# Kernel tuning notes

Hardware: AMD Instinct MI355X
Metric: run time of the kernel (lower is better)

The kernel has to match this reference:

```python
import jax, jax.numpy as jnp
import numpy as np

B, S, H, NH = 8, 1024, 1024, 16
DH = H // NH


def setup_inputs() -> dict:
    key = jax.random.key(0)
    ks = jax.random.split(key, 16)
    inp = {
        'v': jax.random.normal(ks[0], (B, S, H), jnp.float32),
        'k': jax.random.normal(ks[1], (B, S, H), jnp.float32),
        'q': jax.random.normal(ks[2], (B, S, H), jnp.float32),
        'r': jax.random.normal(ks[3], (B, S, H), jnp.float32),
        'mask': jax.random.randint(ks[4], (B, 1, 1, S), 0, 2).astype(jnp.bool_),
    }
    scale = 1.0 / np.sqrt(H)
    names = ['Wv', 'Wk', 'Wq', 'Wr', 'Wm']
    for i, n in enumerate(names):
        inp[n] = jax.random.normal(ks[5 + i], (H, H), jnp.float32) * scale
        inp['b' + n[1:]] = jnp.zeros((H,), jnp.float32)
    return inp


def _heads(x, W, b):
    # torch Linear: x @ W.T + b, then split heads -> [B, NH, S, DH]
    y = jnp.einsum('bsh,oh->bso', x, W) + b
    return y.reshape(B, S, NH, DH).transpose(0, 2, 1, 3)


def reference(v, k, q, r, mask, Wv, bv, Wk, bk, Wq, bq, Wr, br, Wm, bm):
    vh = _heads(v, Wv, bv)
    kh = _heads(k, Wk, bk)
    qh = _heads(q, Wq, bq)
    rh = _heads(r, Wr, br)
    # relation-augmented scores: (QK^T + RK^T) / sqrt(d_k)
    scores = jnp.einsum('bhqd,bhkd->bhqk', qh + rh, kh) / jnp.sqrt(jnp.asarray(DH, qh.dtype))
    scores = jnp.where(mask, jnp.asarray(-1e9, scores.dtype), scores)
    att = jax.nn.softmax(scores, axis=-1)  # dropout = identity in eval
    out = jnp.einsum('bhqk,bhkd->bhqd', att, vh)
    out = out.transpose(0, 2, 1, 3).reshape(B, S, H)
    return jnp.einsum('bsh,oh->bso', out, Wm) + bm
```

## Files before the change

kernel.cpp:

```cpp
#include <hip/hip_runtime.h>
#include <hip/hip_bf16.h>
#include <stdint.h>

typedef __attribute__((ext_vector_type(4))) float f32x4;
typedef __attribute__((ext_vector_type(8))) short s16x8;
typedef __attribute__((ext_vector_type(4))) short s16x4;
typedef __attribute__((ext_vector_type(4))) int i32x4;

typedef const __attribute__((address_space(1))) unsigned glb_u32;
typedef __attribute__((address_space(3))) unsigned lds_u32;

#define DEVI __device__ __forceinline__

DEVI short f2b(float f) {
    union { float f; unsigned u; } v; v.f = f;
    unsigned r = v.u + 0x7fffu + ((v.u >> 16) & 1u);
    return (short)(r >> 16);
}

struct Ptr5 { const float* p[5]; };
struct Ptr4 { const float* p[4]; };

__global__ __launch_bounds__(256) void cvtW(Ptr5 src, short* __restrict__ dst) {
    const float* s = src.p[blockIdx.y];
    short* d = dst + (size_t)blockIdx.y * (1024u * 1024u);
    int i = (blockIdx.x * 256 + threadIdx.x) * 8;
    f32x4 a = *(const f32x4*)(s + i);
    f32x4 b = *(const f32x4*)(s + i + 4);
    s16x8 o;
#pragma unroll
    for (int j = 0; j < 4; ++j) { o[j] = f2b(a[j]); o[4 + j] = f2b(b[j]); }
    *(s16x8*)(d + i) = o;
}

__global__ __launch_bounds__(256) void cvtA(Ptr4 src, short* __restrict__ dst) {
    const float* s = src.p[blockIdx.y];
    short* d = dst + (size_t)blockIdx.y * (8u * 1024u * 1024u);
    int i = (blockIdx.x * 256 + threadIdx.x) * 8;
    f32x4 a = *(const f32x4*)(s + i);
    f32x4 b = *(const f32x4*)(s + i + 4);
    s16x8 o;
#pragma unroll
    for (int j = 0; j < 4; ++j) { o[j] = f2b(a[j]); o[4 + j] = f2b(b[j]); }
    *(s16x8*)(d + i) = o;
}

template<int AF32, int OUTMODE, int TWO>
__global__ __launch_bounds__(256) void gemm_nt(
    const void* __restrict__ A0_, const void* __restrict__ A1_,
    const short* __restrict__ W0, const short* __restrict__ W1,
    const float* __restrict__ b0, const float* __restrict__ b1,
    void* __restrict__ C_)
{
    constexpr int K = 1024, N = 1024;
    const int tid = threadIdx.x;
    const int lane = tid & 63, wid = tid >> 6;
    const int wm = wid >> 1, wn = wid & 1;
    const int r = lane & 15, g = lane >> 4;

    const int bid = blockIdx.x;
    const int logical = (bid & 7) * 64 + (bid >> 3);
    const int n0 = (logical & 7) * 128, m0 = (logical >> 3) * 128;

    __shared__ alignas(16) short As[2][128 * 32];
    __shared__ alignas(16) short Ws[2][128 * 32];

    auto stage_async = [&](int buf, int kt) {
        int kk = kt * 32;
        const short* Ap = (const short*)A0_; const short* Wp = W0;
        if (TWO && kk >= 1024) { Ap = (const short*)A1_; Wp = W1; kk &= 1023; }
#pragma unroll
        for (int i = 0; i < 2; ++i) {
            int row = wid * 32 + i * 16 + (lane >> 2);
            const short* ga = Ap + (size_t)(m0 + row) * K + kk + (lane & 3) * 8;
            const short* gw = Wp + (size_t)(n0 + row) * K + kk + (lane & 3) * 8;
            __builtin_amdgcn_global_load_lds((glb_u32*)ga,
                (lds_u32*)&As[buf][(wid * 32 + i * 16) * 32], 16, 0, 0);
            __builtin_amdgcn_global_load_lds((glb_u32*)gw,
                (lds_u32*)&Ws[buf][(wid * 32 + i * 16) * 32], 16, 0, 0);
        }
    };

    const int srow = tid >> 1, shalf = tid & 1;
    f32x4 a0g, a1g, a2g, a3g;
    s16x8 wg0, wg1;
    auto load_regs = [&](int kt) {
        int kk = kt * 32;
        const short* wp = W0 + (size_t)(n0 + srow) * K + kk + shalf * 16;
        wg0 = *(const s16x8*)wp;
        wg1 = *(const s16x8*)(wp + 8);
        const float* ap = (const float*)A0_ + (size_t)(m0 + srow) * K + kk + shalf * 16;
        a0g = *(const f32x4*)ap;       a1g = *(const f32x4*)(ap + 4);
        a2g = *(const f32x4*)(ap + 8); a3g = *(const f32x4*)(ap + 12);
    };
    auto store_lds = [&](int buf) {
        s16x8 s0, s1;
#pragma unroll
        for (int j = 0; j < 4; ++j) {
            s0[j] = f2b(a0g[j]); s0[4 + j] = f2b(a1g[j]);
            s1[j] = f2b(a2g[j]); s1[4 + j] = f2b(a3g[j]);
        }
        char* ab = (char*)As[buf];
        *(s16x8*)(ab + srow * 64 + shalf * 32) = s0;
        *(s16x8*)(ab + srow * 64 + shalf * 32 + 16) = s1;
        char* wb = (char*)Ws[buf];
        *(s16x8*)(wb + srow * 64 + shalf * 32) = wg0;
        *(s16x8*)(wb + srow * 64 + shalf * 32 + 16) = wg1;
    };

    f32x4 z = {0.f, 0.f, 0.f, 0.f};
    f32x4 acc[4][4];
#pragma unroll
    for (int i = 0; i < 4; ++i)
#pragma unroll
        for (int j = 0; j < 4; ++j) acc[i][j] = z;

    auto compute = [&](int buf) {
        s16x8 af[4], bfr[4];
#pragma unroll
        for (int f = 0; f < 4; ++f) {
            af[f]  = *(const s16x8*)&As[buf][(wm * 64 + f * 16 + r) * 32 + g * 8];
            bfr[f] = *(const s16x8*)&Ws[buf][(wn * 64 + f * 16 + r) * 32 + g * 8];
        }
#pragma unroll
        for (int i = 0; i < 4; ++i)
#pragma unroll
            for (int j = 0; j < 4; ++j)
                acc[i][j] = __builtin_amdgcn_mfma_f32_16x16x32_bf16(af[i], bfr[j], acc[i][j], 0, 0, 0);
    };

    constexpr int NK = TWO ? 64 : 32;
    if constexpr (AF32) { load_regs(0); store_lds(0); }
    else stage_async(0, 0);
    __syncthreads();
    int buf = 0;
    for (int kt = 0; kt < NK; ++kt) {
        if (kt + 1 < NK) {
            if constexpr (AF32) load_regs(kt + 1);
            else stage_async(buf ^ 1, kt + 1);
        }
        compute(buf);
        if (AF32 && kt + 1 < NK) store_lds(buf ^ 1);
        __syncthreads();
        buf ^= 1;
    }

#pragma unroll
    for (int j = 0; j < 4; ++j) {
        int col = n0 + wn * 64 + j * 16 + r;
        float bb = b0[col];
        if (TWO) bb += b1[col];
#pragma unroll
        for (int i = 0; i < 4; ++i) {
            int rowb = m0 + wm * 64 + i * 16 + g * 4;
            if constexpr (OUTMODE == 2) {
                int bb_ = rowb >> 10, tok = rowb & 1023;
                short* dst = (short*)C_ + ((size_t)(bb_ * 16 + (col >> 6))) * 65536
                           + (size_t)(col & 63) * 1024 + tok;
                s16x4 o;
#pragma unroll
                for (int q = 0; q < 4; ++q) o[q] = f2b(acc[i][j][q] + bb);
                *(s16x4*)dst = o;
            } else {
#pragma unroll
                for (int q = 0; q < 4; ++q) {
                    float val = acc[i][j][q] + bb;
                    if constexpr (OUTMODE == 1)
                        ((float*)C_)[(size_t)(rowb + q) * N + col] = val;
                    else
                        ((short*)C_)[(size_t)(rowb + q) * N + col] = f2b(val);
                }
            }
        }
    }
}

__global__ __launch_bounds__(256) void attn_fwd(
    const short* __restrict__ qrh, const short* __restrict__ kh,
    const short* __restrict__ vT, const int* __restrict__ mask,
    short* __restrict__ outp)
{
    const int bh = blockIdx.x;
    const int b = bh >> 4, h = bh & 15;
    const int qt = blockIdx.y;
    const int tid = threadIdx.x, lane = tid & 63, wid = tid >> 6;
    const int r = lane & 15, g = lane >> 4;

    __shared__ alignas(16) short Ks[64 * 64];
    __shared__ alignas(16) short Vs[64 * 64];
    __shared__ alignas(16) float mb[1024];

    {
        i32x4 mi = *(const i32x4*)(mask + b * 1024 + tid * 4);
        f32x4 mv;
#pragma unroll
        for (int j = 0; j < 4; ++j) mv[j] = mi[j] ? -1e9f : 0.f;
        *(f32x4*)&mb[tid * 4] = mv;
    }

    const int q0 = qt * 128 + wid * 32;
    const short* qbA = qrh + (size_t)(b * 1024 + q0 + r) * 1024 + h * 64;
    const short* qbB = qbA + 16 * 1024;
    s16x8 qA0 = *(const s16x8*)(qbA + g * 8);
    s16x8 qA1 = *(const s16x8*)(qbA + 32 + g * 8);
    s16x8 qB0 = *(const s16x8*)(qbB + g * 8);
    s16x8 qB1 = *(const s16x8*)(qbB + 32 + g * 8);

    f32x4 z = {0.f, 0.f, 0.f, 0.f};
    f32x4 oA[4], oB[4];
#pragma unroll
    for (int i = 0; i < 4; ++i) { oA[i] = z; oB[i] = z; }
    float mA = -1e30f, mB = -1e30f, lA = 0.f, lB = 0.f;

    const int srow = tid >> 2, sq = tid & 3;
    const short* kg = kh + (size_t)(b * 1024 + srow) * 1024 + h * 64 + sq * 16;
    const short* vg = vT + ((size_t)(b * 16 + h)) * 65536 + (size_t)srow * 1024 + sq * 16;
    const int p0s = (sq * 2) ^ (srow & 7), p1s = (sq * 2 + 1) ^ (srow & 7);

    s16x8 kr0, kr1, vr0, vr1;
    auto stage_load = [&](int t) {
        const short* kp = kg + (size_t)(t * 64) * 1024;
        kr0 = *(const s16x8*)kp; kr1 = *(const s16x8*)(kp + 8);
        const short* vp = vg + t * 64;
        vr0 = *(const s16x8*)vp; vr1 = *(const s16x8*)(vp + 8);
    };
    auto stage_write = [&]() {
        char* kb2 = (char*)Ks;
        *(s16x8*)(kb2 + srow * 128 + p0s * 16) = kr0;
        *(s16x8*)(kb2 + srow * 128 + p1s * 16) = kr1;
        char* vb2 = (char*)Vs;
        *(s16x8*)(vb2 + srow * 128 + p0s * 16) = vr0;
        *(s16x8*)(vb2 + srow * 128 + p1s * 16) = vr1;
    };

    stage_load(0);
    for (int t = 0; t < 16; ++t) {
        if (t) __syncthreads();
        stage_write();
        __syncthreads();
        if (t < 15) stage_load(t + 1);

        f32x4 pA[4], pB[4];
        float tmA = -3e38f, tmB = -3e38f;
        char* kb2 = (char*)Ks;
#pragma unroll
        for (int fn = 0; fn < 4; ++fn) {
            int row = fn * 16 + r;
            s16x8 kfa = *(const s16x8*)(kb2 + row * 128 + ((g ^ (row & 7)) << 4));
            s16x8 kfb = *(const s16x8*)(kb2 + row * 128 + (((4 + g) ^ (row & 7)) << 4));
            f32x4 cA = __builtin_amdgcn_mfma_f32_16x16x32_bf16(kfa, qA0, z, 0, 0, 0);
            cA = __builtin_amdgcn_mfma_f32_16x16x32_bf16(kfb, qA1, cA, 0, 0, 0);
            f32x4 cB = __builtin_amdgcn_mfma_f32_16x16x32_bf16(kfa, qB0, z, 0, 0, 0);
            cB = __builtin_amdgcn_mfma_f32_16x16x32_bf16(kfb, qB1, cB, 0, 0, 0);
            f32x4 mv = *(const f32x4*)&mb[t * 64 + fn * 16 + g * 4];
#pragma unroll
            for (int qi = 0; qi < 4; ++qi) {
                float sA = cA[qi] * 0.125f + mv[qi];
                float sB = cB[qi] * 0.125f + mv[qi];
                pA[fn][qi] = sA; pB[fn][qi] = sB;
                tmA = fmaxf(tmA, sA); tmB = fmaxf(tmB, sB);
            }
        }
        tmA = fmaxf(tmA, __shfl_xor(tmA, 16)); tmA = fmaxf(tmA, __shfl_xor(tmA, 32));
        tmB = fmaxf(tmB, __shfl_xor(tmB, 16)); tmB = fmaxf(tmB, __shfl_xor(tmB, 32));

        float mnA = fmaxf(mA, tmA), mnB = fmaxf(mB, tmB);
        float cA_ = __expf(mA - mnA), cB_ = __expf(mB - mnB);
        mA = mnA; mB = mnB;
        float tsA = 0.f, tsB = 0.f;
#pragma unroll
        for (int fn = 0; fn < 4; ++fn)
#pragma unroll
            for (int qi = 0; qi < 4; ++qi) {
                float eA = __expf(pA[fn][qi] - mA); pA[fn][qi] = eA; tsA += eA;
                float eB = __expf(pB[fn][qi] - mB); pB[fn][qi] = eB; tsB += eB;
            }
        tsA += __shfl_xor(tsA, 16); tsA += __shfl_xor(tsA, 32);
        tsB += __shfl_xor(tsB, 16); tsB += __shfl_xor(tsB, 32);
        lA = lA * cA_ + tsA; lB = lB * cB_ + tsB;
#pragma unroll
        for (int df = 0; df < 4; ++df)
#pragma unroll
            for (int qi = 0; qi < 4; ++qi) { oA[df][qi] *= cA_; oB[df][qi] *= cB_; }

        char* vb2 = (char*)Vs;
#pragma unroll
        for (int ks = 0; ks < 2; ++ks) {
            s16x8 pbA, pbB;
#pragma unroll
            for (int j = 0; j < 4; ++j) {
                pbA[j]     = f2b(pA[2 * ks][j]);
                pbA[4 + j] = f2b(pA[2 * ks + 1][j]);
                pbB[j]     = f2b(pB[2 * ks][j]);
                pbB[4 + j] = f2b(pB[2 * ks + 1][j]);
            }
#pragma unroll
            for (int df = 0; df < 4; ++df) {
                int row = df * 16 + r;
                int sl0 = ks * 4 + (g >> 1), half = (g & 1) * 8;
                s16x4 va0 = *(const s16x4*)(vb2 + row * 128 + ((sl0 ^ (row & 7)) << 4) + half);
                s16x4 va1 = *(const s16x4*)(vb2 + row * 128 + (((sl0 + 2) ^ (row & 7)) << 4) + half);
                s16x8 vf = {va0[0], va0[1], va0[2], va0[3], va1[0], va1[1], va1[2], va1[3]};
                oA[df] = __builtin_amdgcn_mfma_f32_16x16x32_bf16(vf, pbA, oA[df], 0, 0, 0);
                oB[df] = __builtin_amdgcn_mfma_f32_16x16x32_bf16(vf, pbB, oB[df], 0, 0, 0);
            }
        }
    }

    float ivA = 1.f / lA, ivB = 1.f / lB;
#pragma unroll
    for (int df = 0; df < 4; ++df) {
        s16x4 oa, ob;
#pragma unroll
        for (int qi = 0; qi < 4; ++qi) {
            oa[qi] = f2b(oA[df][qi] * ivA);
            ob[qi] = f2b(oB[df][qi] * ivB);
        }
        *(s16x4*)&outp[(size_t)(b * 1024 + q0 + r) * 1024 + h * 64 + df * 16 + g * 4] = oa;
        *(s16x4*)&outp[(size_t)(b * 1024 + q0 + 16 + r) * 1024 + h * 64 + df * 16 + g * 4] = ob;
    }
}

extern "C" void kernel_launch(void* const* d_in, const int* in_sizes, int n_in,
                              void* d_out, int out_size, void* d_ws, size_t ws_size,
                              hipStream_t stream) {
    const float* v  = (const float*)d_in[0];
    const float* k  = (const float*)d_in[1];
    const float* q  = (const float*)d_in[2];
    const float* rr = (const float*)d_in[3];
    const int* mask = (const int*)d_in[4];
    const float* Wv = (const float*)d_in[5];  const float* bv = (const float*)d_in[6];
    const float* Wk = (const float*)d_in[7];  const float* bk = (const float*)d_in[8];
    const float* Wq = (const float*)d_in[9];  const float* bq = (const float*)d_in[10];
    const float* Wr = (const float*)d_in[11]; const float* br = (const float*)d_in[12];
    const float* Wm = (const float*)d_in[13]; const float* bm = (const float*)d_in[14];

    const size_t MB = 1048576u;
    const size_t NEED_FULL = 90u * MB;
    const size_t NEED_B    = 74u * MB;
    char* ws = (char*)d_ws;
    short* Wb = (short*)ws;

    Ptr5 p5;
    p5.p[0] = Wv; p5.p[1] = Wk; p5.p[2] = Wq; p5.p[3] = Wr; p5.p[4] = Wm;
    cvtW<<<dim3(512, 5), 256, 0, stream>>>(p5, Wb);

    const short* Wvb = Wb, *Wkb = Wb + 1048576u, *Wqb = Wb + 2097152u,
               *Wrb = Wb + 3145728u, *Wmb = Wb + 4194304u;
    dim3 gg(512);

    if (ws_size >= NEED_FULL) {
        short* vb  = (short*)(ws + 10u * MB);
        short* kb  = vb + 8388608u;
        short* qb  = kb + 8388608u;
        short* rb  = qb + 8388608u;
        short* vtb = rb + 8388608u;
        short* khb = vb;
        short* qrb = kb;
        short* att = qb;

        Ptr4 p4; p4.p[0] = v; p4.p[1] = k; p4.p[2] = q; p4.p[3] = rr;
        cvtA<<<dim3(4096, 4), 256, 0, stream>>>(p4, vb);

        gemm_nt<0, 2, 0><<<gg, 256, 0, stream>>>(vb, nullptr, Wvb, nullptr, bv, nullptr, vtb);
        gemm_nt<0, 0, 0><<<gg, 256, 0, stream>>>(kb, nullptr, Wkb, nullptr, bk, nullptr, khb);
        gemm_nt<0, 0, 1><<<gg, 256, 0, stream>>>(qb, rb, Wqb, Wrb, bq, br, qrb);
        attn_fwd<<<dim3(128, 8), 256, 0, stream>>>(qrb, khb, vtb, mask, att);
        gemm_nt<0, 1, 0><<<gg, 256, 0, stream>>>(att, nullptr, Wmb, nullptr, bm, nullptr, (float*)d_out);
    } else if (ws_size >= NEED_B) {
        short* kb  = (short*)(ws + 10u * MB);
        short* qb  = kb + 8388608u;
        short* rb  = qb + 8388608u;
        short* qrb = rb + 8388608u;
        short* vtb = qb;
        short* khb = rb;
        short* att = kb;

        Ptr4 p4; p4.p[0] = k; p4.p[1] = q; p4.p[2] = rr; p4.p[3] = k;
        cvtA<<<dim3(4096, 3), 256, 0, stream>>>(p4, kb);

        gemm_nt<0, 0, 1><<<gg, 256, 0, stream>>>(qb, rb, Wqb, Wrb, bq, br, qrb);
        gemm_nt<1, 2, 0><<<gg, 256, 0, stream>>>(v, nullptr, Wvb, nullptr, bv, nullptr, vtb);
        gemm_nt<0, 0, 0><<<gg, 256, 0, stream>>>(kb, nullptr, Wkb, nullptr, bk, nullptr, khb);
        attn_fwd<<<dim3(128, 8), 256, 0, stream>>>(qrb, khb, vtb, mask, att);
        gemm_nt<0, 1, 0><<<gg, 256, 0, stream>>>(att, nullptr, Wmb, nullptr, bm, nullptr, (float*)d_out);
    }
}
```

Baseline: 253.3 us.

## Use exp2 softmax, packed bf16 converts, and permuted V layout for single LDS reads

New measurement: 242.6 us. -4.2%, faster.

```diff
diff --git a/kernel.cpp b/kernel.cpp
--- a/kernel.cpp
+++ b/kernel.cpp
@@ -17,6 +17,36 @@
     unsigned r = v.u + 0x7fffu + ((v.u >> 16) & 1u);
     return (short)(r >> 16);
 }
+
+DEVI float vexp2(float x) {
+    float r;
+    asm("v_exp_f32 %0, %1" : "=v"(r) : "v"(x));
+    return r;
+}
+
+DEVI float vmax3(float a, float b, float c) {
+    float d;
+    asm("v_max3_f32 %0, %1, %2, %3" : "=v"(d) : "v"(a), "v"(b), "v"(c));
+    return d;
+}
+
+DEVI unsigned cvtpk(float lo, float hi) {
+    unsigned d;
+    asm("v_cvt_pk_bf16_f32 %0, %1, %2" : "=v"(d) : "v"(lo), "v"(hi));
+    return d;
+}
+
+DEVI s16x8 pack8(const f32x4& a, const f32x4& b) {
+    union { unsigned u[4]; s16x8 v; } w;
+    w.u[0] = cvtpk(a[0], a[1]);
+    w.u[1] = cvtpk(a[2], a[3]);
+    w.u[2] = cvtpk(b[0], b[1]);
+    w.u[3] = cvtpk(b[2], b[3]);
+    return w.v;
+}
+
+#define QSCL 0.18033688011112042f
+#define MASKV -1.4426950408889634e9f
 
 struct Ptr5 { const float* p[5]; };
 struct Ptr4 { const float* p[4]; };
@@ -155,8 +185,9 @@
             int rowb = m0 + wm * 64 + i * 16 + g * 4;
             if constexpr (OUTMODE == 2) {
                 int bb_ = rowb >> 10, tok = rowb & 1023;
+                int tokp = (tok & ~31) | (((tok >> 2) & 3) << 3) | (((tok >> 4) & 1) << 2);
                 short* dst = (short*)C_ + ((size_t)(bb_ * 16 + (col >> 6))) * 65536
-                           + (size_t)(col & 63) * 1024 + tok;
+                           + (size_t)(col & 63) * 1024 + tokp;
                 s16x4 o;
 #pragma unroll
                 for (int q = 0; q < 4; ++q) o[q] = f2b(acc[i][j][q] + bb);
@@ -194,7 +225,7 @@
         i32x4 mi = *(const i32x4*)(mask + b * 1024 + tid * 4);
         f32x4 mv;
 #pragma unroll
-        for (int j = 0; j < 4; ++j) mv[j] = mi[j] ? -1e9f : 0.f;
+        for (int j = 0; j < 4; ++j) mv[j] = mi[j] ? MASKV : 0.f;
         *(f32x4*)&mb[tid * 4] = mv;
     }
 
@@ -255,25 +286,27 @@
             f32x4 mv = *(const f32x4*)&mb[t * 64 + fn * 16 + g * 4];
 #pragma unroll
             for (int qi = 0; qi < 4; ++qi) {
-                float sA = cA[qi] * 0.125f + mv[qi];
-                float sB = cB[qi] * 0.125f + mv[qi];
-                pA[fn][qi] = sA; pB[fn][qi] = sB;
-                tmA = fmaxf(tmA, sA); tmB = fmaxf(tmB, sB);
+                pA[fn][qi] = cA[qi] * QSCL + mv[qi];
+                pB[fn][qi] = cB[qi] * QSCL + mv[qi];
             }
+            tmA = vmax3(tmA, pA[fn][0], pA[fn][1]);
+            tmA = vmax3(tmA, pA[fn][2], pA[fn][3]);
+            tmB = vmax3(tmB, pB[fn][0], pB[fn][1]);
+            tmB = vmax3(tmB, pB[fn][2], pB[fn][3]);
         }
         tmA = fmaxf(tmA, __shfl_xor(tmA, 16)); tmA = fmaxf(tmA, __shfl_xor(tmA, 32));
         tmB = fmaxf(tmB, __shfl_xor(tmB, 16)); tmB = fmaxf(tmB, __shfl_xor(tmB, 32));
 
         float mnA = fmaxf(mA, tmA), mnB = fmaxf(mB, tmB);
-        float cA_ = __expf(mA - mnA), cB_ = __expf(mB - mnB);
+        float cA_ = vexp2(mA - mnA), cB_ = vexp2(mB - mnB);
         mA = mnA; mB = mnB;
         float tsA = 0.f, tsB = 0.f;
 #pragma unroll
         for (int fn = 0; fn < 4; ++fn)
 #pragma unroll
             for (int qi = 0; qi < 4; ++qi) {
-                float eA = __expf(pA[fn][qi] - mA); pA[fn][qi] = eA; tsA += eA;
-                float eB = __expf(pB[fn][qi] - mB); pB[fn][qi] = eB; tsB += eB;
+                float eA = vexp2(pA[fn][qi] - mA); pA[fn][qi] = eA; tsA += eA;
+                float eB = vexp2(pB[fn][qi] - mB); pB[fn][qi] = eB; tsB += eB;
             }
         tsA += __shfl_xor(tsA, 16); tsA += __shfl_xor(tsA, 32);
         tsB += __shfl_xor(tsB, 16); tsB += __shfl_xor(tsB, 32);
@@ -286,21 +319,13 @@
         char* vb2 = (char*)Vs;
 #pragma unroll
         for (int ks = 0; ks < 2; ++ks) {
-            s16x8 pbA, pbB;
-#pragma unroll
-            for (int j = 0; j < 4; ++j) {
-                pbA[j]     = f2b(pA[2 * ks][j]);
-                pbA[4 + j] = f2b(pA[2 * ks + 1][j]);
-                pbB[j]     = f2b(pB[2 * ks][j]);
-                pbB[4 + j] = f2b(pB[2 * ks + 1][j]);
-            }
+            s16x8 pbA = pack8(pA[2 * ks], pA[2 * ks + 1]);
+            s16x8 pbB = pack8(pB[2 * ks], pB[2 * ks + 1]);
 #pragma unroll
             for (int df = 0; df < 4; ++df) {
                 int row = df * 16 + r;
-                int sl0 = ks * 4 + (g >> 1), half = (g & 1) * 8;
-                s16x4 va0 = *(const s16x4*)(vb2 + row * 128 + ((sl0 ^ (row & 7)) << 4) + half);
-                s16x4 va1 = *(const s16x4*)(vb2 + row * 128 + (((sl0 + 2) ^ (row & 7)) << 4) + half);
-                s16x8 vf = {va0[0], va0[1], va0[2], va0[3], va1[0], va1[1], va1[2], va1[3]};
+                int slot = (ks * 4 + g) ^ (row & 7);
+                s16x8 vf = *(const s16x8*)(vb2 + row * 128 + (slot << 4));
                 oA[df] = __builtin_amdgcn_mfma_f32_16x16x32_bf16(vf, pbA, oA[df], 0, 0, 0);
                 oB[df] = __builtin_amdgcn_mfma_f32_16x16x32_bf16(vf, pbB, oB[df], 0, 0, 0);
             }
```
